# Performance work log

Measured on AMD Instinct MI355X. Metric: run time of the kernel, lower is better.

The kernel has to match this reference:

```python
import jax, jax.numpy as jnp
import numpy as np

B, S, E, H, V, CV = 128, 1024, 256, 512, 128, 101
PAD = 100  # cipher pad idx -> zero embedding row


def setup_inputs() -> dict:
    key = jax.random.key(0)
    ks = jax.random.split(key, 12)
    stdv = 1.0 / np.sqrt(H)
    u = lambda k, shp, s: jax.random.uniform(k, shp, jnp.float32, -s, s)
    emb = jax.random.normal(ks[0], (CV, E), jnp.float32)
    emb = emb.at[PAD].set(0.0)  # padding_idx row zeroed
    out_s = 1.0 / np.sqrt(H)    # nn.Linear default init scale
    return {
        "x": jax.random.randint(ks[1], (B, S), 0, 100),
        "emb": emb,
        "W_ih0": u(ks[2], (H, E), stdv), "b_ih0": u(ks[3], (H,), stdv),
        "W_hh0": u(ks[4], (H, H), stdv), "b_hh0": u(ks[5], (H,), stdv),
        "W_ih1": u(ks[6], (H, H), stdv), "b_ih1": u(ks[7], (H,), stdv),
        "W_hh1": u(ks[8], (H, H), stdv), "b_hh1": u(ks[9], (H,), stdv),
        "W_out": u(ks[10], (V, H), out_s), "b_out": u(ks[11], (V,), out_s),
    }


def reference(x, emb, W_ih0, b_ih0, W_hh0, b_hh0, W_ih1, b_ih1, W_hh1, b_hh1, W_out, b_out):
    # eval mode: dropout is identity
    embeds = emb[x]                      # (B, S, E)
    h0 = jnp.zeros((x.shape[0], H), embeds.dtype)
    h1 = jnp.zeros((x.shape[0], H), embeds.dtype)

    def step(carry, xt):
        h0, h1 = carry
        h0n = jnp.tanh(xt @ W_ih0.T + b_ih0 + h0 @ W_hh0.T + b_hh0)
        h1n = jnp.tanh(h0n @ W_ih1.T + b_ih1 + h1 @ W_hh1.T + b_hh1)
        return (h0n, h1n), h1n

    (h0f, h1f), outs = jax.lax.scan(step, (h0, h1), embeds.swapaxes(0, 1))  # outs: (S, B, H)
    output = outs.swapaxes(0, 1)                   # (B, S, H)
    logits = output @ W_out.T + b_out              # (B, S, V)
    h_n = jnp.stack([h0f, h1f], axis=0)            # (2, B, H)
    return logits, h_n
```

## Files before the change

### kernel.cpp

```cpp
#include <hip/hip_runtime.h>

constexpr int B = 128, S = 1024, E = 256, H = 512, V = 128;
constexpr int NGROUP = 8, WPG = 15, NWG = 128;
constexpr int GB = B / NGROUP;
constexpr int NT = 512;
constexpr unsigned LDS_BYTES = 32768;

using short8 = __attribute__((ext_vector_type(8))) short;
using f32x4  = __attribute__((ext_vector_type(4))) float;
using u16    = unsigned short;

#define MFMA_B16(a, b, c) __builtin_amdgcn_mfma_f32_16x16x32_bf16((a), (b), (c), 0, 0, 0)

__device__ __forceinline__ unsigned pk(float a, float b) {
  return (__builtin_bit_cast(unsigned, b) & 0xFFFF0000u) |
         (__builtin_bit_cast(unsigned, a) >> 16);
}
__device__ __forceinline__ float hif(float a) {
  return __builtin_bit_cast(float, __builtin_bit_cast(unsigned, a) & 0xFFFF0000u);
}
__device__ __forceinline__ void cvt16(const float4& v0, const float4& v1,
                                      const float4& v2, const float4& v3,
                                      uint4& h0, uint4& h1, uint4& l0, uint4& l1) {
  h0 = make_uint4(pk(v0.x, v0.y), pk(v0.z, v0.w), pk(v1.x, v1.y), pk(v1.z, v1.w));
  h1 = make_uint4(pk(v2.x, v2.y), pk(v2.z, v2.w), pk(v3.x, v3.y), pk(v3.z, v3.w));
  l0 = make_uint4(pk(v0.x - hif(v0.x), v0.y - hif(v0.y)),
                  pk(v0.z - hif(v0.z), v0.w - hif(v0.w)),
                  pk(v1.x - hif(v1.x), v1.y - hif(v1.y)),
                  pk(v1.z - hif(v1.z), v1.w - hif(v1.w)));
  l1 = make_uint4(pk(v2.x - hif(v2.x), v2.y - hif(v2.y)),
                  pk(v2.z - hif(v2.z), v2.w - hif(v2.w)),
                  pk(v3.x - hif(v3.x), v3.y - hif(v3.y)),
                  pk(v3.z - hif(v3.z), v3.w - hif(v3.w)));
}

__device__ __forceinline__ float ftanh(float x) {
  float e = __expf(2.0f * x);
  return 1.0f - 2.0f * __builtin_amdgcn_rcpf(e + 1.0f);
}

__device__ __forceinline__ void stg_sys_f32(float* p, float v) {
  asm volatile("global_store_dword %0, %1, off sc0 sc1" :: "v"(p), "v"(v) : "memory");
}
__device__ __forceinline__ void stg_sys_u32(unsigned* p, unsigned v) {
  asm volatile("global_store_dword %0, %1, off sc0 sc1" :: "v"(p), "v"(v) : "memory");
}
__device__ __forceinline__ void stg_sys_u16(u16* p, unsigned v) {
  asm volatile("global_store_short %0, %1, off sc0 sc1" :: "v"(p), "v"(v) : "memory");
}

__device__ __forceinline__ void gbar(unsigned* slots, int r, unsigned target, int tid) {
  asm volatile("s_waitcnt vmcnt(0)" ::: "memory");
  __syncthreads();
  if (tid < 64) {
    if (tid == 0)
      asm volatile("global_store_dword %0, %1, off sc0 sc1"
                   :: "v"(slots + r), "v"(target) : "memory");
    for (;;) {
      unsigned v = target;
      if (tid < WPG)
        asm volatile("global_load_dword %0, %1, off sc0 sc1\n\ts_waitcnt vmcnt(0)"
                     : "=v"(v) : "v"(slots + tid) : "memory");
      if (__all((int)(v >= target))) break;
      __builtin_amdgcn_s_sleep(1);
    }
  }
  __syncthreads();
}

template <int KK>
__device__ __forceinline__ void loadWfrag(const float* W, int col0, int lane,
                                          short8* wh, short8* wl) {
  const int lc = col0 + (lane & 15);
  const int q = lane >> 4;
#pragma unroll
  for (int ks = 0; ks < KK / 32; ++ks) {
    const float* src = W + (size_t)lc * KK + ks * 32 + q * 8;
    float4 a = *(const float4*)src;
    float4 b = *(const float4*)(src + 4);
    uint4 h = make_uint4(pk(a.x, a.y), pk(a.z, a.w), pk(b.x, b.y), pk(b.z, b.w));
    uint4 l = make_uint4(pk(a.x - hif(a.x), a.y - hif(a.y)),
                         pk(a.z - hif(a.z), a.w - hif(a.w)),
                         pk(b.x - hif(b.x), b.y - hif(b.y)),
                         pk(b.z - hif(b.z), b.w - hif(b.w)));
    wh[ks] = __builtin_bit_cast(short8, h);
    wl[ks] = __builtin_bit_cast(short8, l);
  }
}

__device__ __forceinline__ void compute_offs(int tid, int* off, int* lof) {
#pragma unroll
  for (int it = 0; it < 2; ++it) {
    int s = tid + it * NT, rr = s >> 6, ks = s & 63;
    off[it] = rr * 1024 + ks * 16;
    lof[it] = off[it] ^ ((rr & 7) << 4);
  }
}
__device__ __forceinline__ void stage4(int tid, const u16* Ph, const u16* Pl,
                                       char* AH, char* AL) {
  int off[2], lof[2];
  compute_offs(tid, off, lof);
  const char* gh = (const char*)Ph;
  const char* gl = (const char*)Pl;
  float4 o0, o1, o2, o3;
  asm volatile(
      "global_load_dwordx4 %0, %4, off sc0 sc1\n\t"
      "global_load_dwordx4 %1, %5, off sc0 sc1\n\t"
      "global_load_dwordx4 %2, %6, off sc0 sc1\n\t"
      "global_load_dwordx4 %3, %7, off sc0 sc1\n\t"
      "s_waitcnt vmcnt(0)"
      : "=&v"(o0), "=&v"(o1), "=&v"(o2), "=&v"(o3)
      : "v"(gh + off[0]), "v"(gh + off[1]), "v"(gl + off[0]), "v"(gl + off[1])
      : "memory");
  *(float4*)(AH + lof[0]) = o0; *(float4*)(AH + lof[1]) = o1;
  *(float4*)(AL + lof[0]) = o2; *(float4*)(AL + lof[1]) = o3;
}
__device__ __forceinline__ void stage8i(int tid, const u16* Ph, const u16* Pl,
                                        char* AH, char* AL,
                                        const float* q0, const float* q1,
                                        const float* q2, const float* q3,
                                        float& i0, float& i1, float& i2, float& i3) {
  int off[2], lof[2];
  compute_offs(tid, off, lof);
  const char* gh = (const char*)Ph;
  const char* gl = (const char*)Pl;
  float4 o0, o1, o2, o3;
  asm volatile(
      "global_load_dword %4, %12, off sc0 sc1\n\t"
      "global_load_dword %5, %13, off sc0 sc1\n\t"
      "global_load_dword %6, %14, off sc0 sc1\n\t"
      "global_load_dword %7, %15, off sc0 sc1\n\t"
      "global_load_dwordx4 %0, %8, off sc0 sc1\n\t"
      "global_load_dwordx4 %1, %9, off sc0 sc1\n\t"
      "global_load_dwordx4 %2, %10, off sc0 sc1\n\t"
      "global_load_dwordx4 %3, %11, off sc0 sc1\n\t"
      "s_waitcnt vmcnt(0)"
      : "=&v"(o0), "=&v"(o1), "=&v"(o2), "=&v"(o3),
        "=&v"(i0), "=&v"(i1), "=&v"(i2), "=&v"(i3)
      : "v"(gh + off[0]), "v"(gh + off[1]), "v"(gl + off[0]), "v"(gl + off[1]),
        "v"(q0), "v"(q1), "v"(q2), "v"(q3)
      : "memory");
  *(float4*)(AH + lof[0]) = o0; *(float4*)(AH + lof[1]) = o1;
  *(float4*)(AL + lof[0]) = o2; *(float4*)(AL + lof[1]) = o3;
}

template <int KK>
__device__ __forceinline__ f32x4 mm_frag_reg(const char* AH, const char* AL,
                                             const short8* wh, const short8* wl,
                                             int lane) {
  constexpr int ROWB = KK * 2;
  const int rr = lane & 15;
  const int kq = (lane >> 4) * 16;
  const int swa = (rr & 7) << 4;
  f32x4 a0 = {0.f, 0.f, 0.f, 0.f}, a1 = {0.f, 0.f, 0.f, 0.f};
#pragma unroll
  for (int ks = 0; ks < KK / 32; ++ks) {
    int ka = rr * ROWB + ks * 64 + kq;
    short8 ah = *(const short8*)(AH + (ka ^ swa));
    short8 al = *(const short8*)(AL + (ka ^ swa));
    a0 = MFMA_B16(ah, wh[ks], a0);
    a1 = MFMA_B16(ah, wl[ks], a1);
    a1 = MFMA_B16(al, wh[ks], a1);
  }
  return a0 + a1;
}

__device__ __forceinline__ void run_h(
    int tid, int lane, int w, unsigned* slots, int r, int dt,
    u16* hh, u16* hl, const float* imb, float* hn2base,
    const float* Wsrc, int tn, char* AH, char* AL) {
  short8 wh[16], wl[16];
  loadWfrag<512>(Wsrc, tn * 128 + w * 16, lane, wh, wl);
  gbar(slots, r, 1, tid);
  const int lc15 = lane & 15, r0 = (lane >> 4) * 4;
  const int gcol = tn * 128 + w * 16 + lc15;
  for (int p = 0; p <= S + 3; ++p) {
    int t = p - dt;
    if (t >= 0 && t < S) {
      const u16* Ph = hh + ((t - 1) & 1) * 8192;
      const u16* Pl = hl + ((t - 1) & 1) * 8192;
      const float* iq = imb + (t & 1) * 8192 + (size_t)r0 * H + gcol;
      float i0, i1, i2, i3;
      stage8i(tid, Ph, Pl, AH, AL, iq, iq + H, iq + 2 * H, iq + 3 * H, i0, i1, i2, i3);
      __syncthreads();
      f32x4 s = mm_frag_reg<512>(AH, AL, wh, wl, lane);
      u16* Dh = hh + (t & 1) * 8192;
      u16* Dl = hl + (t & 1) * 8192;
      float iv[4] = {i0, i1, i2, i3};
      bool last = (t == S - 1);
#pragma unroll
      for (int j = 0; j < 4; ++j) {
        float v = ftanh(s[j] + iv[j]);
        unsigned ub = __builtin_bit_cast(unsigned, v);
        float lov = v - __builtin_bit_cast(float, ub & 0xFFFF0000u);
        stg_sys_u16(Dh + (size_t)(r0 + j) * H + gcol, ub >> 16);
        stg_sys_u16(Dl + (size_t)(r0 + j) * H + gcol,
                    __builtin_bit_cast(unsigned, lov) >> 16);
        if (last) hn2base[(size_t)(r0 + j) * H + gcol] = v;
      }
    }
    gbar(slots, r, 2 + p, tid);
  }
}

__device__ __forceinline__ void run_g(
    int tid, int lane, int w, unsigned* slots, int r,
    const u16* h0h, const u16* h0l, float* Gg,
    const float* b1, const float* b2,
    const float* Wsrc, int tn, char* AH, char* AL) {
  short8 wh[16], wl[16];
  loadWfrag<512>(Wsrc, tn * 128 + w * 16, lane, wh, wl);
  gbar(slots, r, 1, tid);
  const int lc15 = lane & 15, r0 = (lane >> 4) * 4;
  const int gcol = tn * 128 + w * 16 + lc15;
  const float bsum = b1[gcol] + b2[gcol];
  for (int p = 0; p <= S + 3; ++p) {
    int t = p - 2;
    if (t >= 0 && t < S) {
      stage4(tid, h0h + (t & 1) * 8192, h0l + (t & 1) * 8192, AH, AL);
      __syncthreads();
      f32x4 s = mm_frag_reg<512>(AH, AL, wh, wl, lane);
      float* D = Gg + (t & 1) * 8192;
#pragma unroll
      for (int j = 0; j < 4; ++j)
        stg_sys_f32(D + (size_t)(r0 + j) * H + gcol, s[j] + bsum);
    }
    gbar(slots, r, 2 + p, tid);
  }
}

__device__ __forceinline__ void run_ain(
    int tid, int lane, int w, unsigned* slots, int r,
    const int* x, const float* emb, float* Ain,
    const float* b1, const float* b2,
    const float* Wsrc, int a, int gb0, char* AH, char* AL) {
  short8 whA[8], wlA[8], whB[8], wlB[8];
  const int col0 = a * 256 + w * 32;
  loadWfrag<256>(Wsrc, col0, lane, whA, wlA);
  loadWfrag<256>(Wsrc, col0 + 16, lane, whB, wlB);
  gbar(slots, r, 1, tid);
  const int lc15 = lane & 15, r0 = (lane >> 4) * 4;
  const int gcolA = col0 + lc15, gcolB = gcolA + 16;
  const float bsA = b1[gcolA] + b2[gcolA], bsB = b1[gcolB] + b2[gcolB];
  const int rr = tid >> 4, q = tid & 15;
  for (int p = 0; p <= S + 3; ++p) {
    int t = p;
    if (t < S) {
      if (tid < 256) {
        int idx = x[(size_t)(gb0 + rr) * S + t];
        const float4* src = (const float4*)(emb + (size_t)idx * E + q * 16);
        float4 v0 = src[0], v1 = src[1], v2 = src[2], v3 = src[3];
        uint4 h0v, h1v, l0v, l1v;
        cvt16(v0, v1, v2, v3, h0v, h1v, l0v, l1v);
        int bb = rr * 512 + q * 32, sw = (rr & 7) << 4;
        *(uint4*)(AH + ((bb) ^ sw)) = h0v;
        *(uint4*)(AH + ((bb + 16) ^ sw)) = h1v;
        *(uint4*)(AL + ((bb) ^ sw)) = l0v;
        *(uint4*)(AL + ((bb + 16) ^ sw)) = l1v;
      }
      __syncthreads();
      f32x4 sA = mm_frag_reg<256>(AH, AL, whA, wlA, lane);
      f32x4 sB = mm_frag_reg<256>(AH, AL, whB, wlB, lane);
      float* D = Ain + (t & 1) * 8192;
#pragma unroll
      for (int j = 0; j < 4; ++j) {
        stg_sys_f32(D + (size_t)(r0 + j) * H + gcolA, sA[j] + bsA);
        stg_sys_f32(D + (size_t)(r0 + j) * H + gcolB, sB[j] + bsB);
      }
    }
    gbar(slots, r, 2 + p, tid);
  }
}

__device__ __forceinline__ void run_out(
    int tid, int lane, int w, unsigned* slots, int r,
    const u16* h1h, const u16* h1l, float* out, const float* b_out,
    const float* Wsrc, int gb0, char* AH, char* AL) {
  short8 wh[16], wl[16];
  loadWfrag<512>(Wsrc, w * 16, lane, wh, wl);
  gbar(slots, r, 1, tid);
  const int lc15 = lane & 15, r0 = (lane >> 4) * 4;
  const int gcol = w * 16 + lc15;
  const float bv = b_out[gcol];
  for (int p = 0; p <= S + 3; ++p) {
    int t = p - 4;
    if (t >= 0 && t < S) {
      stage4(tid, h1h + (t & 1) * 8192, h1l + (t & 1) * 8192, AH, AL);
      __syncthreads();
      f32x4 s = mm_frag_reg<512>(AH, AL, wh, wl, lane);
#pragma unroll
      for (int j = 0; j < 4; ++j)
        out[((size_t)(gb0 + r0 + j) * S + t) * V + gcol] = s[j] + bv;
    }
    gbar(slots, r, 2 + p, tid);
  }
}

__global__ void __launch_bounds__(NT, 1) rnn_pers(
    const int* __restrict__ x, const float* __restrict__ emb,
    const float* __restrict__ W_ih0, const float* __restrict__ b_ih0,
    const float* __restrict__ W_hh0, const float* __restrict__ b_hh0,
    const float* __restrict__ W_ih1, const float* __restrict__ b_ih1,
    const float* __restrict__ W_hh1, const float* __restrict__ b_hh1,
    const float* __restrict__ W_out, const float* __restrict__ b_out,
    float* __restrict__ out, float* __restrict__ ws)
{
  extern __shared__ char lds[];
  char* AH = lds;
  char* AL = lds + 16384;

  const int tid = threadIdx.x;
  const int g = blockIdx.x >> 4;
  const int r = blockIdx.x & 15;
  if (r >= WPG) return;

  unsigned* slots = (unsigned*)ws + (size_t)g * 64;
  float* base = ws + 1024 + (size_t)g * 65536;
  float* Ain = base;
  float* Gg  = base + 16384;
  u16* h0h = (u16*)(base + 32768);
  u16* h0l = h0h + 16384;
  u16* h1h = h0h + 32768;
  u16* h1l = h0h + 49152;
  const int gb0 = g * GB;

  {
    unsigned* zp = (unsigned*)h0h;
    for (int i = r * NT + tid; i < 32768; i += WPG * NT) stg_sys_u32(zp + i, 0u);
  }

  const int lane = tid & 63, w = tid >> 6;
  float* hn = out + (size_t)B * S * V;

  if (r < 4)
    run_h(tid, lane, w, slots, r, 1, h0h, h0l, Ain,
          hn + (size_t)gb0 * H, W_hh0, r, AH, AL);
  else if (r < 8)
    run_g(tid, lane, w, slots, r, h0h, h0l, Gg, b_ih1, b_hh1,
          W_ih1, r - 4, AH, AL);
  else if (r < 12)
    run_h(tid, lane, w, slots, r, 3, h1h, h1l, Gg,
          hn + (size_t)B * H + (size_t)gb0 * H, W_hh1, r - 8, AH, AL);
  else if (r < 14)
    run_ain(tid, lane, w, slots, r, x, emb, Ain, b_ih0, b_hh0,
            W_ih0, r - 12, gb0, AH, AL);
  else
    run_out(tid, lane, w, slots, r, h1h, h1l, out, b_out,
            W_out, gb0, AH, AL);
}

extern "C" void kernel_launch(void* const* d_in, const int* in_sizes, int n_in,
                              void* d_out, int out_size, void* d_ws, size_t ws_size,
                              hipStream_t stream) {
  const int*   x     = (const int*)d_in[0];
  const float* emb   = (const float*)d_in[1];
  const float* W_ih0 = (const float*)d_in[2];
  const float* b_ih0 = (const float*)d_in[3];
  const float* W_hh0 = (const float*)d_in[4];
  const float* b_hh0 = (const float*)d_in[5];
  const float* W_ih1 = (const float*)d_in[6];
  const float* b_ih1 = (const float*)d_in[7];
  const float* W_hh1 = (const float*)d_in[8];
  const float* b_hh1 = (const float*)d_in[9];
  const float* W_out = (const float*)d_in[10];
  const float* b_out = (const float*)d_in[11];
  float* out = (float*)d_out;
  float* ws  = (float*)d_ws;

  hipFuncSetAttribute((const void*)rnn_pers,
                      hipFuncAttributeMaxDynamicSharedMemorySize, (int)LDS_BYTES);
  hipMemsetAsync(ws, 0, 4096, stream);

  void* args[] = { &x, &emb, &W_ih0, &b_ih0, &W_hh0, &b_hh0, &W_ih1, &b_ih1,
                   &W_hh1, &b_hh1, &W_out, &b_out, &out, &ws };
  hipLaunchCooperativeKernel((const void*)rnn_pers, dim3(NWG), dim3(NT),
                             args, LDS_BYTES, stream);
}
```

Measured before the change: 3.728 ms.

## Halve batch groups, fuse input projection into layer-0 recurrence, shorten pipeline

Halves the number of batch groups, so each workgroup handles 32 rows instead of 16 and runs two MFMA row tiles per weight fragment. The embedding input projection (W_ih0) moves into the layer-0 recurrence workgroups, which stage each timestep's embeddings in LDS. This removes the separate Ain producer stage and one pipeline step. The aim is to cut the number of per-step grid barriers and the Ain round trip through global memory, at the cost of more work per workgroup on the serial critical path and larger LDS use.

Measured after the change: 9.485 ms. 2.54x slower.

```diff
diff --git a/kernel.cpp b/kernel.cpp
--- a/kernel.cpp
+++ b/kernel.cpp
@@ -1,10 +1,10 @@
 #include <hip/hip_runtime.h>
 
 constexpr int B = 128, S = 1024, E = 256, H = 512, V = 128;
-constexpr int NGROUP = 8, WPG = 15, NWG = 128;
+constexpr int NGROUP = 4, WPG = 13, NWG = 64;
 constexpr int GB = B / NGROUP;
 constexpr int NT = 512;
-constexpr unsigned LDS_BYTES = 32768;
+constexpr unsigned LDS_BYTES = 98304;
 
 using short8 = __attribute__((ext_vector_type(8))) short;
 using f32x4  = __attribute__((ext_vector_type(4))) float;
@@ -88,209 +88,282 @@
   }
 }
 
-__device__ __forceinline__ void compute_offs(int tid, int* off, int* lof) {
-#pragma unroll
-  for (int it = 0; it < 2; ++it) {
+__device__ __forceinline__ void stage16(int tid, const u16* Ph, const u16* Pl,
+                                        char* AH, char* AL) {
+  int off[4], lof[4];
+#pragma unroll
+  for (int it = 0; it < 4; ++it) {
     int s = tid + it * NT, rr = s >> 6, ks = s & 63;
     off[it] = rr * 1024 + ks * 16;
     lof[it] = off[it] ^ ((rr & 7) << 4);
   }
-}
-__device__ __forceinline__ void stage4(int tid, const u16* Ph, const u16* Pl,
-                                       char* AH, char* AL) {
-  int off[2], lof[2];
-  compute_offs(tid, off, lof);
   const char* gh = (const char*)Ph;
   const char* gl = (const char*)Pl;
-  float4 o0, o1, o2, o3;
+  float4 a0, a1, a2, a3, b0, b1, b2, b3;
   asm volatile(
-      "global_load_dwordx4 %0, %4, off sc0 sc1\n\t"
-      "global_load_dwordx4 %1, %5, off sc0 sc1\n\t"
-      "global_load_dwordx4 %2, %6, off sc0 sc1\n\t"
-      "global_load_dwordx4 %3, %7, off sc0 sc1\n\t"
-      "s_waitcnt vmcnt(0)"
-      : "=&v"(o0), "=&v"(o1), "=&v"(o2), "=&v"(o3)
-      : "v"(gh + off[0]), "v"(gh + off[1]), "v"(gl + off[0]), "v"(gl + off[1])
-      : "memory");
-  *(float4*)(AH + lof[0]) = o0; *(float4*)(AH + lof[1]) = o1;
-  *(float4*)(AL + lof[0]) = o2; *(float4*)(AL + lof[1]) = o3;
-}
-__device__ __forceinline__ void stage8i(int tid, const u16* Ph, const u16* Pl,
-                                        char* AH, char* AL,
-                                        const float* q0, const float* q1,
-                                        const float* q2, const float* q3,
-                                        float& i0, float& i1, float& i2, float& i3) {
-  int off[2], lof[2];
-  compute_offs(tid, off, lof);
-  const char* gh = (const char*)Ph;
-  const char* gl = (const char*)Pl;
-  float4 o0, o1, o2, o3;
-  asm volatile(
-      "global_load_dword %4, %12, off sc0 sc1\n\t"
-      "global_load_dword %5, %13, off sc0 sc1\n\t"
-      "global_load_dword %6, %14, off sc0 sc1\n\t"
-      "global_load_dword %7, %15, off sc0 sc1\n\t"
       "global_load_dwordx4 %0, %8, off sc0 sc1\n\t"
       "global_load_dwordx4 %1, %9, off sc0 sc1\n\t"
       "global_load_dwordx4 %2, %10, off sc0 sc1\n\t"
       "global_load_dwordx4 %3, %11, off sc0 sc1\n\t"
+      "global_load_dwordx4 %4, %12, off sc0 sc1\n\t"
+      "global_load_dwordx4 %5, %13, off sc0 sc1\n\t"
+      "global_load_dwordx4 %6, %14, off sc0 sc1\n\t"
+      "global_load_dwordx4 %7, %15, off sc0 sc1\n\t"
       "s_waitcnt vmcnt(0)"
-      : "=&v"(o0), "=&v"(o1), "=&v"(o2), "=&v"(o3),
-        "=&v"(i0), "=&v"(i1), "=&v"(i2), "=&v"(i3)
-      : "v"(gh + off[0]), "v"(gh + off[1]), "v"(gl + off[0]), "v"(gl + off[1]),
-        "v"(q0), "v"(q1), "v"(q2), "v"(q3)
+      : "=&v"(a0), "=&v"(a1), "=&v"(a2), "=&v"(a3),
+        "=&v"(b0), "=&v"(b1), "=&v"(b2), "=&v"(b3)
+      : "v"(gh + off[0]), "v"(gh + off[1]), "v"(gh + off[2]), "v"(gh + off[3]),
+        "v"(gl + off[0]), "v"(gl + off[1]), "v"(gl + off[2]), "v"(gl + off[3])
       : "memory");
-  *(float4*)(AH + lof[0]) = o0; *(float4*)(AH + lof[1]) = o1;
-  *(float4*)(AL + lof[0]) = o2; *(float4*)(AL + lof[1]) = o3;
+  *(float4*)(AH + lof[0]) = a0; *(float4*)(AH + lof[1]) = a1;
+  *(float4*)(AH + lof[2]) = a2; *(float4*)(AH + lof[3]) = a3;
+  *(float4*)(AL + lof[0]) = b0; *(float4*)(AL + lof[1]) = b1;
+  *(float4*)(AL + lof[2]) = b2; *(float4*)(AL + lof[3]) = b3;
+}
+
+__device__ __forceinline__ void stage16i(int tid, const u16* Ph, const u16* Pl,
+                                         char* AH, char* AL,
+                                         const float* q0, const float* q2,
+                                         const float* q16, const float* q18,
+                                         float* iw) {
+  int off[4], lof[4];
+#pragma unroll
+  for (int it = 0; it < 4; ++it) {
+    int s = tid + it * NT, rr = s >> 6, ks = s & 63;
+    off[it] = rr * 1024 + ks * 16;
+    lof[it] = off[it] ^ ((rr & 7) << 4);
+  }
+  const char* gh = (const char*)Ph;
+  const char* gl = (const char*)Pl;
+  float4 a0, a1, a2, a3, b0, b1, b2, b3;
+  asm volatile(
+      "global_load_dword %8, %20, off sc0 sc1\n\t"
+      "global_load_dword %9, %20, off offset:2048 sc0 sc1\n\t"
+      "global_load_dword %10, %21, off sc0 sc1\n\t"
+      "global_load_dword %11, %21, off offset:2048 sc0 sc1\n\t"
+      "global_load_dword %12, %22, off sc0 sc1\n\t"
+      "global_load_dword %13, %22, off offset:2048 sc0 sc1\n\t"
+      "global_load_dword %14, %23, off sc0 sc1\n\t"
+      "global_load_dword %15, %23, off offset:2048 sc0 sc1\n\t"
+      "global_load_dwordx4 %0, %16, off sc0 sc1\n\t"
+      "global_load_dwordx4 %1, %17, off sc0 sc1\n\t"
+      "global_load_dwordx4 %2, %18, off sc0 sc1\n\t"
+      "global_load_dwordx4 %3, %19, off sc0 sc1\n\t"
+      "global_load_dwordx4 %4, %24, off sc0 sc1\n\t"
+      "global_load_dwordx4 %5, %25, off sc0 sc1\n\t"
+      "global_load_dwordx4 %6, %26, off sc0 sc1\n\t"
+      "global_load_dwordx4 %7, %27, off sc0 sc1\n\t"
+      "s_waitcnt vmcnt(0)"
+      : "=&v"(a0), "=&v"(a1), "=&v"(a2), "=&v"(a3),
+        "=&v"(b0), "=&v"(b1), "=&v"(b2), "=&v"(b3),
+        "=&v"(iw[0]), "=&v"(iw[1]), "=&v"(iw[2]), "=&v"(iw[3]),
+        "=&v"(iw[4]), "=&v"(iw[5]), "=&v"(iw[6]), "=&v"(iw[7])
+      : "v"(gh + off[0]), "v"(gh + off[1]), "v"(gh + off[2]), "v"(gh + off[3]),
+        "v"(q0), "v"(q2), "v"(q16), "v"(q18),
+        "v"(gl + off[0]), "v"(gl + off[1]), "v"(gl + off[2]), "v"(gl + off[3])
+      : "memory");
+  *(float4*)(AH + lof[0]) = a0; *(float4*)(AH + lof[1]) = a1;
+  *(float4*)(AH + lof[2]) = a2; *(float4*)(AH + lof[3]) = a3;
+  *(float4*)(AL + lof[0]) = b0; *(float4*)(AL + lof[1]) = b1;
+  *(float4*)(AL + lof[2]) = b2; *(float4*)(AL + lof[3]) = b3;
 }
 
 template <int KK>
-__device__ __forceinline__ f32x4 mm_frag_reg(const char* AH, const char* AL,
-                                             const short8* wh, const short8* wl,
-                                             int lane) {
+__device__ __forceinline__ void mm2(const char* AH, const char* AL,
+                                    const short8* wh, const short8* wl,
+                                    int lane, f32x4& s0h, f32x4& s0l,
+                                    f32x4& s1h, f32x4& s1l) {
   constexpr int ROWB = KK * 2;
   const int rr = lane & 15;
   const int kq = (lane >> 4) * 16;
   const int swa = (rr & 7) << 4;
-  f32x4 a0 = {0.f, 0.f, 0.f, 0.f}, a1 = {0.f, 0.f, 0.f, 0.f};
 #pragma unroll
   for (int ks = 0; ks < KK / 32; ++ks) {
-    int ka = rr * ROWB + ks * 64 + kq;
-    short8 ah = *(const short8*)(AH + (ka ^ swa));
-    short8 al = *(const short8*)(AL + (ka ^ swa));
-    a0 = MFMA_B16(ah, wh[ks], a0);
-    a1 = MFMA_B16(ah, wl[ks], a1);
-    a1 = MFMA_B16(al, wh[ks], a1);
-  }
-  return a0 + a1;
-}
-
-__device__ __forceinline__ void run_h(
-    int tid, int lane, int w, unsigned* slots, int r, int dt,
-    u16* hh, u16* hl, const float* imb, float* hn2base,
-    const float* Wsrc, int tn, char* AH, char* AL) {
-  short8 wh[16], wl[16];
-  loadWfrag<512>(Wsrc, tn * 128 + w * 16, lane, wh, wl);
-  gbar(slots, r, 1, tid);
+    int ka0 = rr * ROWB + ks * 64 + kq;
+    int ka1 = ka0 + 16 * ROWB;
+    short8 ah0 = *(const short8*)(AH + (ka0 ^ swa));
+    short8 al0 = *(const short8*)(AL + (ka0 ^ swa));
+    short8 ah1 = *(const short8*)(AH + (ka1 ^ swa));
+    short8 al1 = *(const short8*)(AL + (ka1 ^ swa));
+    s0h = MFMA_B16(ah0, wh[ks], s0h);
+    s0l = MFMA_B16(ah0, wl[ks], s0l);
+    s0l = MFMA_B16(al0, wh[ks], s0l);
+    s1h = MFMA_B16(ah1, wh[ks], s1h);
+    s1l = MFMA_B16(ah1, wl[ks], s1l);
+    s1l = MFMA_B16(al1, wh[ks], s1l);
+  }
+}
+
+__device__ void run_h0(int tid, int lane, int w, unsigned* slots, int r,
+                       u16* hh, u16* hl, const int* x, const float* emb,
+                       const float* b1, const float* b2, float* hnb,
+                       const float* Whh, const float* Wih, int tn, int gb0,
+                       char* AH, char* AL, char* EH, char* EL) {
+  short8 whh[16], wlh[16], whi[8], wli[8];
+  loadWfrag<512>(Whh, tn * 128 + w * 16, lane, whh, wlh);
+  loadWfrag<256>(Wih, tn * 128 + w * 16, lane, whi, wli);
   const int lc15 = lane & 15, r0 = (lane >> 4) * 4;
   const int gcol = tn * 128 + w * 16 + lc15;
-  for (int p = 0; p <= S + 3; ++p) {
-    int t = p - dt;
-    if (t >= 0 && t < S) {
-      const u16* Ph = hh + ((t - 1) & 1) * 8192;
-      const u16* Pl = hl + ((t - 1) & 1) * 8192;
-      const float* iq = imb + (t & 1) * 8192 + (size_t)r0 * H + gcol;
-      float i0, i1, i2, i3;
-      stage8i(tid, Ph, Pl, AH, AL, iq, iq + H, iq + 2 * H, iq + 3 * H, i0, i1, i2, i3);
+  const float bsum = b1[gcol] + b2[gcol];
+  const int er = tid >> 4, eq = tid & 15;
+  {
+    int idx = x[(size_t)(gb0 + er) * S + 0];
+    const float4* src = (const float4*)(emb + (size_t)idx * E + eq * 16);
+    float4 v0 = src[0], v1 = src[1], v2 = src[2], v3 = src[3];
+    uint4 h0v, h1v, l0v, l1v;
+    cvt16(v0, v1, v2, v3, h0v, h1v, l0v, l1v);
+    int bb = er * 512 + eq * 32, sw = (er & 7) << 4;
+    *(uint4*)(EH + (bb ^ sw)) = h0v; *(uint4*)(EH + ((bb + 16) ^ sw)) = h1v;
+    *(uint4*)(EL + (bb ^ sw)) = l0v; *(uint4*)(EL + ((bb + 16) ^ sw)) = l1v;
+  }
+  gbar(slots, r, 1, tid);
+  for (int p = 0; p <= S + 2; ++p) {
+    int t = p;
+    if (t < S) {
+      stage16(tid, hh + ((t - 1) & 1) * 16384, hl + ((t - 1) & 1) * 16384, AH, AL);
       __syncthreads();
-      f32x4 s = mm_frag_reg<512>(AH, AL, wh, wl, lane);
-      u16* Dh = hh + (t & 1) * 8192;
-      u16* Dl = hl + (t & 1) * 8192;
-      float iv[4] = {i0, i1, i2, i3};
-      bool last = (t == S - 1);
+      f32x4 s0h = {0,0,0,0}, s0l = {0,0,0,0}, s1h = {0,0,0,0}, s1l = {0,0,0,0};
+      mm2<512>(AH, AL, whh, wlh, lane, s0h, s0l, s1h, s1l);
+      mm2<256>(EH, EL, whi, wli, lane, s0h, s0l, s1h, s1l);
+      f32x4 s0 = s0h + s0l, s1 = s1h + s1l;
+      u16* Dh = hh + (t & 1) * 16384;
+      u16* Dl = hl + (t & 1) * 16384;
+      const bool last = (t == S - 1);
 #pragma unroll
       for (int j = 0; j < 4; ++j) {
-        float v = ftanh(s[j] + iv[j]);
+        float v = ftanh(s0[j] + bsum);
         unsigned ub = __builtin_bit_cast(unsigned, v);
         float lov = v - __builtin_bit_cast(float, ub & 0xFFFF0000u);
-        stg_sys_u16(Dh + (size_t)(r0 + j) * H + gcol, ub >> 16);
-        stg_sys_u16(Dl + (size_t)(r0 + j) * H + gcol,
+        int row = r0 + j;
+        stg_sys_u16(Dh + (size_t)row * H + gcol, ub >> 16);
+        stg_sys_u16(Dl + (size_t)row * H + gcol,
                     __builtin_bit_cast(unsigned, lov) >> 16);
-        if (last) hn2base[(size_t)(r0 + j) * H + gcol] = v;
+        if (last) hnb[(size_t)row * H + gcol] = v;
+        float v2 = ftanh(s1[j] + bsum);
+        unsigned ub2 = __builtin_bit_cast(unsigned, v2);
+        float lov2 = v2 - __builtin_bit_cast(float, ub2 & 0xFFFF0000u);
+        int row2 = r0 + 16 + j;
+        stg_sys_u16(Dh + (size_t)row2 * H + gcol, ub2 >> 16);
+        stg_sys_u16(Dl + (size_t)row2 * H + gcol,
+                    __builtin_bit_cast(unsigned, lov2) >> 16);
+        if (last) hnb[(size_t)row2 * H + gcol] = v2;
+      }
+      if (t + 1 < S) {
+        __syncthreads();
+        int idx = x[(size_t)(gb0 + er) * S + (t + 1)];
+        const float4* src = (const float4*)(emb + (size_t)idx * E + eq * 16);
+        float4 v0 = src[0], v1 = src[1], v2 = src[2], v3 = src[3];
+        uint4 h0v, h1v, l0v, l1v;
+        cvt16(v0, v1, v2, v3, h0v, h1v, l0v, l1v);
+        int bb = er * 512 + eq * 32, sw = (er & 7) << 4;
+        *(uint4*)(EH + (bb ^ sw)) = h0v; *(uint4*)(EH + ((bb + 16) ^ sw)) = h1v;
+        *(uint4*)(EL + (bb ^ sw)) = l0v; *(uint4*)(EL + ((bb + 16) ^ sw)) = l1v;
       }
     }
     gbar(slots, r, 2 + p, tid);
   }
 }
 
-__device__ __forceinline__ void run_g(
-    int tid, int lane, int w, unsigned* slots, int r,
-    const u16* h0h, const u16* h0l, float* Gg,
-    const float* b1, const float* b2,
-    const float* Wsrc, int tn, char* AH, char* AL) {
+__device__ void run_g(int tid, int lane, int w, unsigned* slots, int r,
+                      const u16* h0h, const u16* h0l, float* Gg,
+                      const float* b1, const float* b2,
+                      const float* Wsrc, int tn, char* AH, char* AL) {
   short8 wh[16], wl[16];
   loadWfrag<512>(Wsrc, tn * 128 + w * 16, lane, wh, wl);
   gbar(slots, r, 1, tid);
   const int lc15 = lane & 15, r0 = (lane >> 4) * 4;
   const int gcol = tn * 128 + w * 16 + lc15;
   const float bsum = b1[gcol] + b2[gcol];
-  for (int p = 0; p <= S + 3; ++p) {
-    int t = p - 2;
+  for (int p = 0; p <= S + 2; ++p) {
+    int t = p - 1;
     if (t >= 0 && t < S) {
-      stage4(tid, h0h + (t & 1) * 8192, h0l + (t & 1) * 8192, AH, AL);
+      stage16(tid, h0h + (t & 1) * 16384, h0l + (t & 1) * 16384, AH, AL);
       __syncthreads();
-      f32x4 s = mm_frag_reg<512>(AH, AL, wh, wl, lane);
-      float* D = Gg + (t & 1) * 8192;
-#pragma unroll
-      for (int j = 0; j < 4; ++j)
-        stg_sys_f32(D + (size_t)(r0 + j) * H + gcol, s[j] + bsum);
-    }
-    gbar(slots, r, 2 + p, tid);
-  }
-}
-
-__device__ __forceinline__ void run_ain(
-    int tid, int lane, int w, unsigned* slots, int r,
-    const int* x, const float* emb, float* Ain,
-    const float* b1, const float* b2,
-    const float* Wsrc, int a, int gb0, char* AH, char* AL) {
-  short8 whA[8], wlA[8], whB[8], wlB[8];
-  const int col0 = a * 256 + w * 32;
-  loadWfrag<256>(Wsrc, col0, lane, whA, wlA);
-  loadWfrag<256>(Wsrc, col0 + 16, lane, whB, wlB);
-  gbar(slots, r, 1, tid);
-  const int lc15 = lane & 15, r0 = (lane >> 4) * 4;
-  const int gcolA = col0 + lc15, gcolB = gcolA + 16;
-  const float bsA = b1[gcolA] + b2[gcolA], bsB = b1[gcolB] + b2[gcolB];
-  const int rr = tid >> 4, q = tid & 15;
-  for (int p = 0; p <= S + 3; ++p) {
-    int t = p;
-    if (t < S) {
-      if (tid < 256) {
-        int idx = x[(size_t)(gb0 + rr) * S + t];
-        const float4* src = (const float4*)(emb + (size_t)idx * E + q * 16);
-        float4 v0 = src[0], v1 = src[1], v2 = src[2], v3 = src[3];
-        uint4 h0v, h1v, l0v, l1v;
-        cvt16(v0, v1, v2, v3, h0v, h1v, l0v, l1v);
-        int bb = rr * 512 + q * 32, sw = (rr & 7) << 4;
-        *(uint4*)(AH + ((bb) ^ sw)) = h0v;
-        *(uint4*)(AH + ((bb + 16) ^ sw)) = h1v;
-        *(uint4*)(AL + ((bb) ^ sw)) = l0v;
-        *(uint4*)(AL + ((bb + 16) ^ sw)) = l1v;
-      }
-      __syncthreads();
-      f32x4 sA = mm_frag_reg<256>(AH, AL, whA, wlA, lane);
-      f32x4 sB = mm_frag_reg<256>(AH, AL, whB, wlB, lane);
-      float* D = Ain + (t & 1) * 8192;
+      f32x4 s0h = {0,0,0,0}, s0l = {0,0,0,0}, s1h = {0,0,0,0}, s1l = {0,0,0,0};
+      mm2<512>(AH, AL, wh, wl, lane, s0h, s0l, s1h, s1l);
+      f32x4 s0 = s0h + s0l, s1 = s1h + s1l;
+      float* D = Gg + (t & 1) * 16384;
 #pragma unroll
       for (int j = 0; j < 4; ++j) {
-        stg_sys_f32(D + (size_t)(r0 + j) * H + gcolA, sA[j] + bsA);
-        stg_sys_f32(D + (size_t)(r0 + j) * H + gcolB, sB[j] + bsB);
+        stg_sys_f32(D + (size_t)(r0 + j) * H + gcol, s0[j] + bsum);
+        stg_sys_f32(D + (size_t)(r0 + 16 + j) * H + gcol, s1[j] + bsum);
       }
     }
     gbar(slots, r, 2 + p, tid);
   }
 }
 
-__device__ __forceinline__ void run_out(
-    int tid, int lane, int w, unsigned* slots, int r,
-    const u16* h1h, const u16* h1l, float* out, const float* b_out,
-    const float* Wsrc, int gb0, char* AH, char* AL) {
+__device__ void run_h1(int tid, int lane, int w, unsigned* slots, int r,
+                       u16* hh, u16* hl, const float* Gg, float* hnb,
+                       const float* Wsrc, int tn, char* AH, char* AL) {
+  short8 wh[16], wl[16];
+  loadWfrag<512>(Wsrc, tn * 128 + w * 16, lane, wh, wl);
+  gbar(slots, r, 1, tid);
+  const int lc15 = lane & 15, r0 = (lane >> 4) * 4;
+  const int gcol = tn * 128 + w * 16 + lc15;
+  for (int p = 0; p <= S + 2; ++p) {
+    int t = p - 2;
+    if (t >= 0 && t < S) {
+      const float* iq = Gg + (t & 1) * 16384 + (size_t)r0 * H + gcol;
+      float iw[8];
+      stage16i(tid, hh + ((t - 1) & 1) * 16384, hl + ((t - 1) & 1) * 16384,
+               AH, AL, iq, iq + 2 * H, iq + 16 * H, iq + 18 * H, iw);
+      __syncthreads();
+      f32x4 s0h = {0,0,0,0}, s0l = {0,0,0,0}, s1h = {0,0,0,0}, s1l = {0,0,0,0};
+      mm2<512>(AH, AL, wh, wl, lane, s0h, s0l, s1h, s1l);
+      f32x4 s0 = s0h + s0l, s1 = s1h + s1l;
+      u16* Dh = hh + (t & 1) * 16384;
+      u16* Dl = hl + (t & 1) * 16384;
+      const bool last = (t == S - 1);
+#pragma unroll
+      for (int j = 0; j < 4; ++j) {
+        float v = ftanh(s0[j] + iw[2 * j]);
+        float v2 = ftanh(s1[j] + iw[2 * j + 1]);
+        v  = ftanh(s0[j] + iw[j]);
+        v2 = ftanh(s1[j] + iw[4 + j]);
+        unsigned ub = __builtin_bit_cast(unsigned, v);
+        float lov = v - __builtin_bit_cast(float, ub & 0xFFFF0000u);
+        int row = r0 + j;
+        stg_sys_u16(Dh + (size_t)row * H + gcol, ub >> 16);
+        stg_sys_u16(Dl + (size_t)row * H + gcol,
+                    __builtin_bit_cast(unsigned, lov) >> 16);
+        if (last) hnb[(size_t)row * H + gcol] = v;
+        unsigned ub2 = __builtin_bit_cast(unsigned, v2);
+        float lov2 = v2 - __builtin_bit_cast(float, ub2 & 0xFFFF0000u);
+        int row2 = r0 + 16 + j;
+        stg_sys_u16(Dh + (size_t)row2 * H + gcol, ub2 >> 16);
+        stg_sys_u16(Dl + (size_t)row2 * H + gcol,
+                    __builtin_bit_cast(unsigned, lov2) >> 16);
+        if (last) hnb[(size_t)row2 * H + gcol] = v2;
+      }
+    }
+    gbar(slots, r, 2 + p, tid);
+  }
+}
+
+__device__ void run_out(int tid, int lane, int w, unsigned* slots, int r,
+                        const u16* h1h, const u16* h1l, float* out,
+                        const float* b_out, const float* Wsrc, int gb0,
+                        char* AH, char* AL) {
   short8 wh[16], wl[16];
   loadWfrag<512>(Wsrc, w * 16, lane, wh, wl);
   gbar(slots, r, 1, tid);
   const int lc15 = lane & 15, r0 = (lane >> 4) * 4;
   const int gcol = w * 16 + lc15;
   const float bv = b_out[gcol];
-  for (int p = 0; p <= S + 3; ++p) {
-    int t = p - 4;
+  for (int p = 0; p <= S + 2; ++p) {
+    int t = p - 3;
     if (t >= 0 && t < S) {
-      stage4(tid, h1h + (t & 1) * 8192, h1l + (t & 1) * 8192, AH, AL);
+      stage16(tid, h1h + (t & 1) * 16384, h1l + (t & 1) * 16384, AH, AL);
       __syncthreads();
-      f32x4 s = mm_frag_reg<512>(AH, AL, wh, wl, lane);
-#pragma unroll
-      for (int j = 0; j < 4; ++j)
-        out[((size_t)(gb0 + r0 + j) * S + t) * V + gcol] = s[j] + bv;
+      f32x4 s0h = {0,0,0,0}, s0l = {0,0,0,0}, s1h = {0,0,0,0}, s1l = {0,0,0,0};
+      mm2<512>(AH, AL, wh, wl, lane, s0h, s0l, s1h, s1l);
+      f32x4 s0 = s0h + s0l, s1 = s1h + s1l;
+#pragma unroll
+      for (int j = 0; j < 4; ++j) {
+        out[((size_t)(gb0 + r0 + j) * S + t) * V + gcol] = s0[j] + bv;
+        out[((size_t)(gb0 + r0 + 16 + j) * S + t) * V + gcol] = s1[j] + bv;
+      }
     }
     gbar(slots, r, 2 + p, tid);
   }
@@ -307,7 +380,9 @@
 {
   extern __shared__ char lds[];
   char* AH = lds;
-  char* AL = lds + 16384;
+  char* AL = lds + 32768;
+  char* EH = lds + 65536;
+  char* EL = lds + 81920;
 
   const int tid = threadIdx.x;
   const int g = blockIdx.x >> 4;
@@ -315,38 +390,33 @@
   if (r >= WPG) return;
 
   unsigned* slots = (unsigned*)ws + (size_t)g * 64;
-  float* base = ws + 1024 + (size_t)g * 65536;
-  float* Ain = base;
-  float* Gg  = base + 16384;
+  float* base = ws + 1024 + (size_t)g * 98304;
+  float* Gg = base;
   u16* h0h = (u16*)(base + 32768);
-  u16* h0l = h0h + 16384;
-  u16* h1h = h0h + 32768;
-  u16* h1l = h0h + 49152;
+  u16* h0l = h0h + 32768;
+  u16* h1h = h0h + 65536;
+  u16* h1l = h0h + 98304;
   const int gb0 = g * GB;
 
   {
     unsigned* zp = (unsigned*)h0h;
-    for (int i = r * NT + tid; i < 32768; i += WPG * NT) stg_sys_u32(zp + i, 0u);
+    for (int i = r * NT + tid; i < 65536; i += WPG * NT) stg_sys_u32(zp + i, 0u);
   }
 
   const int lane = tid & 63, w = tid >> 6;
   float* hn = out + (size_t)B * S * V;
 
   if (r < 4)
-    run_h(tid, lane, w, slots, r, 1, h0h, h0l, Ain,
-          hn + (size_t)gb0 * H, W_hh0, r, AH, AL);
+    run_h0(tid, lane, w, slots, r, h0h, h0l, x, emb, b_ih0, b_hh0,
+           hn + (size_t)gb0 * H, W_hh0, W_ih0, r, gb0, AH, AL, EH, EL);
   else if (r < 8)
     run_g(tid, lane, w, slots, r, h0h, h0l, Gg, b_ih1, b_hh1,
           W_ih1, r - 4, AH, AL);
   else if (r < 12)
-    run_h(tid, lane, w, slots, r, 3, h1h, h1l, Gg,
-          hn + (size_t)B * H + (size_t)gb0 * H, W_hh1, r - 8, AH, AL);
-  else if (r < 14)
-    run_ain(tid, lane, w, slots, r, x, emb, Ain, b_ih0, b_hh0,
-            W_ih0, r - 12, gb0, AH, AL);
+    run_h1(tid, lane, w, slots, r, h1h, h1l, Gg,
+           hn + (size_t)B * H + (size_t)gb0 * H, W_hh1, r - 8, AH, AL);
   else
-    run_out(tid, lane, w, slots, r, h1h, h1l, out, b_out,
-            W_out, gb0, AH, AL);
+    run_out(tid, lane, w, slots, r, h1h, h1l, out, b_out, W_out, gb0, AH, AL);
 }
 
 extern "C" void kernel_launch(void* const* d_in, const int* in_sizes, int n_in,
```
